# Optimization experiments

Hardware: AMD Instinct MI355X
Metric: run time of the kernel (lower is better)

## Reference

```python
import jax, jax.numpy as jnp
import numpy as np

B, N, CIN, COUT = 2, 4096, 128, 64

def setup_inputs() -> dict:
    key = jax.random.key(0)
    ks = jax.random.split(key, 9)
    s1 = 1.0 / np.sqrt(CIN)
    s2 = 1.0 / np.sqrt(COUT)
    sa = 1.0 / np.sqrt(2 * COUT)
    return {
        "x": jax.random.normal(ks[0], (B, N, CIN), dtype=jnp.float32),
        "adj_matrix": jax.random.uniform(ks[1], (B, N, N), dtype=jnp.float32),
        "W1": jax.random.uniform(ks[2], (CIN, COUT), jnp.float32, -s1, s1),
        "b1": jax.random.uniform(ks[3], (COUT,), jnp.float32, -s1, s1),
        "W2": jax.random.uniform(ks[4], (COUT, COUT), jnp.float32, -s2, s2),
        "b2": jax.random.uniform(ks[5], (COUT,), jnp.float32, -s2, s2),
        "Wa": jax.random.uniform(ks[6], (2 * COUT, 1), jnp.float32, -sa, sa),
        "ba": jax.random.uniform(ks[7], (1,), jnp.float32, -sa, sa),
    }

def reference(x, adj_matrix, W1, b1, W2, b2, Wa, ba):
    # conv: two Linear+ReLU layers -> h [B,N,C]
    h = jax.nn.relu(jnp.einsum('bni,io->bno', x, W1) + b1)
    h = jax.nn.relu(jnp.einsum('bni,io->bno', h, W2) + b2)
    # attention Linear(2C,1) on cat[h_i, h_j] factorizes: e_ij = sigmoid(u_i + v_j + b)
    C = h.shape[-1]
    u = jnp.einsum('bnc,c->bn', h, Wa[:C, 0])  # contribution of node i (row)
    v = jnp.einsum('bnc,c->bn', h, Wa[C:, 0])  # contribution of node j (col)
    e = jax.nn.sigmoid(u[:, :, None] + v[:, None, :] + ba[0])  # [B,N,N]
    a = e * adj_matrix
    a = a / (jnp.sum(a, axis=-1, keepdims=True) + 1e-10)
    h_out = jnp.einsum('bnm,bmc->bnc', a, h)
    return (h_out, a)
```

## Files before the change

### kernel.cpp

```cpp
#include <hip/hip_runtime.h>

#define BB 2
#define NN 4096
#define CIN 128
#define CC 64

typedef __attribute__((ext_vector_type(4))) float floatx4;
typedef __attribute__((ext_vector_type(8))) short short8;

__device__ __forceinline__ short f2bf(float f) {
    unsigned u = __float_as_uint(f);
    u += 0x7fffu + ((u >> 16) & 1u);
    return (short)(u >> 16);
}

__device__ __forceinline__ float sigf(float x) {
    return __builtin_amdgcn_rcpf(1.0f + __expf(-x));
}

__global__ __launch_bounds__(256) void feat_v3(
    const float* __restrict__ x, const float* __restrict__ W1,
    const float* __restrict__ b1, const float* __restrict__ W2,
    const float* __restrict__ b2, const float* __restrict__ Wa,
    const float* __restrict__ ba,
    short* __restrict__ hT, float* __restrict__ u, float* __restrict__ v)
{
    __shared__ float W1s[CIN * CC];
    __shared__ float W2s[CC * CC];
    __shared__ float xs[16 * 132];
    __shared__ float h1s[16 * 68];
    __shared__ __align__(16) short hs[CC][16];

    const int t = threadIdx.x;
    const int row0 = blockIdx.x * 16;

    {
        const floatx4* s1 = (const floatx4*)W1;
        floatx4* d1 = (floatx4*)W1s;
        for (int i = t; i < CIN * CC / 4; i += 256) d1[i] = s1[i];
        const floatx4* s2 = (const floatx4*)W2;
        floatx4* d2 = (floatx4*)W2s;
        for (int i = t; i < CC * CC / 4; i += 256) d2[i] = s2[i];
        const floatx4* sx = (const floatx4*)(x + (size_t)row0 * CIN);
        for (int i = t; i < 16 * CIN / 4; i += 256) {
            int rw = i >> 5, c4 = i & 31;
            *(floatx4*)(xs + rw * 132 + c4 * 4) = sx[i];
        }
    }
    __syncthreads();

    const int n  = t >> 4;
    const int cg = t & 15;
    const int c0 = cg * 4;

    float acc[4];
#pragma unroll
    for (int i = 0; i < 4; i++) acc[i] = b1[c0 + i];
    for (int k = 0; k < CIN; k++) {
        float a = xs[n * 132 + k];
        const floatx4 w = *(const floatx4*)&W1s[k * CC + c0];
#pragma unroll
        for (int i = 0; i < 4; i++) acc[i] = fmaf(a, w[i], acc[i]);
    }
#pragma unroll
    for (int i = 0; i < 4; i++) h1s[n * 68 + c0 + i] = fmaxf(acc[i], 0.0f);
    __syncthreads();

    float acc2[4];
#pragma unroll
    for (int i = 0; i < 4; i++) acc2[i] = b2[c0 + i];
    for (int k = 0; k < CC; k++) {
        float a = h1s[n * 68 + k];
        const floatx4 w = *(const floatx4*)&W2s[k * CC + c0];
#pragma unroll
        for (int i = 0; i < 4; i++) acc2[i] = fmaf(a, w[i], acc2[i]);
    }
#pragma unroll
    for (int i = 0; i < 4; i++) acc2[i] = fmaxf(acc2[i], 0.0f);

#pragma unroll
    for (int i = 0; i < 4; i++) hs[c0 + i][n] = f2bf(acc2[i]);

    float pu = 0.0f, pv = 0.0f;
#pragma unroll
    for (int i = 0; i < 4; i++) {
        pu = fmaf(acc2[i], Wa[c0 + i], pu);
        pv = fmaf(acc2[i], Wa[CC + c0 + i], pv);
    }
    pu += __shfl_down(pu, 8, 16); pv += __shfl_down(pv, 8, 16);
    pu += __shfl_down(pu, 4, 16); pv += __shfl_down(pv, 4, 16);
    pu += __shfl_down(pu, 2, 16); pv += __shfl_down(pv, 2, 16);
    pu += __shfl_down(pu, 1, 16); pv += __shfl_down(pv, 1, 16);

    const int grow = row0 + n;
    if (cg == 0) { u[grow] = pu + ba[0]; v[grow] = pv; }

    __syncthreads();
    if (t < 128) {
        const int c  = t >> 1;
        const int hf = t & 1;
        const int b   = row0 >> 12;
        const int nn0 = row0 & (NN - 1);
        *(short8*)(hT + ((size_t)(b * CC + c)) * NN + nn0 + hf * 8) =
            *(const short8*)&hs[c][hf * 8];
    }
}

__global__ __launch_bounds__(256, 2) void attn_v3(
    const float* __restrict__ adj, const float* __restrict__ u,
    const float* __restrict__ v, const short* __restrict__ hT,
    float* __restrict__ hout, float* __restrict__ aout)
{
    __shared__ float red[4][16][CC + 1];
    __shared__ float rsum[4][16];
    __shared__ float rinv[16];

    const int wave = threadIdx.x >> 6;
    const int lane = threadIdx.x & 63;
    const int row0 = blockIdx.x * 16;
    const int b  = row0 >> 12;
    const int n0 = row0 & (NN - 1);
    const float* vb = v + b * NN;
    const int jw = wave * 1024;

    float psum[16];
    {
        floatx4 vA = *(const floatx4*)(vb + jw +       lane * 4);
        floatx4 vB = *(const floatx4*)(vb + jw + 256 + lane * 4);
        floatx4 vC = *(const floatx4*)(vb + jw + 512 + lane * 4);
        floatx4 vD = *(const floatx4*)(vb + jw + 768 + lane * 4);
#pragma unroll 4
        for (int r = 0; r < 16; ++r) {
            const float* ar = adj + ((size_t)(b * NN + n0 + r)) * NN + jw;
            floatx4 aA = *(const floatx4*)(ar +       lane * 4);
            floatx4 aB = *(const floatx4*)(ar + 256 + lane * 4);
            floatx4 aC = *(const floatx4*)(ar + 512 + lane * 4);
            floatx4 aD = *(const floatx4*)(ar + 768 + lane * 4);
            const float ur = u[b * NN + n0 + r];
            float p = 0.f;
#pragma unroll
            for (int i = 0; i < 4; ++i) {
                p = fmaf(aA[i], sigf(ur + vA[i]), p);
                p = fmaf(aB[i], sigf(ur + vB[i]), p);
                p = fmaf(aC[i], sigf(ur + vC[i]), p);
                p = fmaf(aD[i], sigf(ur + vD[i]), p);
            }
            psum[r] = p;
        }
    }
#pragma unroll
    for (int off = 32; off; off >>= 1) {
#pragma unroll
        for (int r = 0; r < 16; ++r) psum[r] += __shfl_down(psum[r], off);
    }
    if (lane == 0) {
#pragma unroll
        for (int r = 0; r < 16; ++r) rsum[wave][r] = psum[r];
    }
    __syncthreads();
    if (threadIdx.x < 16) {
        const int r = threadIdx.x;
        float s = rsum[0][r] + rsum[1][r] + rsum[2][r] + rsum[3][r];
        rinv[r] = __builtin_amdgcn_rcpf(s + 1e-10f);
    }
    __syncthreads();

    const int quad = lane >> 4;
    const int m16  = lane & 15;
    const int n    = n0 + m16;
    const size_t rowbase = ((size_t)(b * NN + n)) * NN;
    const float un    = u[b * NN + n];
    const float inv_r = rinv[m16];

    const float* ap_base = adj + rowbase;
    float*       op_base = aout + rowbase;
    const short* hp0 = hT + ((size_t)(b * CC +  0 + m16)) * NN;
    const short* hp1 = hT + ((size_t)(b * CC + 16 + m16)) * NN;
    const short* hp2 = hT + ((size_t)(b * CC + 32 + m16)) * NN;
    const short* hp3 = hT + ((size_t)(b * CC + 48 + m16)) * NN;

    floatx4 acc[4];
#pragma unroll
    for (int g = 0; g < 4; g++) acc[g] = (floatx4){0.f, 0.f, 0.f, 0.f};

    const int jb0 = jw + quad * 8;

    floatx4 a0A, a1A, v0A, v1A; short8 h0A, h1A, h2A, h3A;
    floatx4 a0B, a1B, v0B, v1B; short8 h0B, h1B, h2B, h3B;

#define LOADST(S, jb) { \
    a0##S = *(const floatx4*)(ap_base + (jb));      \
    a1##S = *(const floatx4*)(ap_base + (jb) + 4);  \
    v0##S = *(const floatx4*)(vb + (jb));           \
    v1##S = *(const floatx4*)(vb + (jb) + 4);       \
    h0##S = *(const short8*)(hp0 + (jb));           \
    h1##S = *(const short8*)(hp1 + (jb));           \
    h2##S = *(const short8*)(hp2 + (jb));           \
    h3##S = *(const short8*)(hp3 + (jb)); }

#define COMPST(S, jb) { \
    float av[8] = {a0##S.x, a0##S.y, a0##S.z, a0##S.w, a1##S.x, a1##S.y, a1##S.z, a1##S.w}; \
    float vv[8] = {v0##S.x, v0##S.y, v0##S.z, v0##S.w, v1##S.x, v1##S.y, v1##S.z, v1##S.w}; \
    floatx4 o0, o1; short8 af; \
    _Pragma("unroll") \
    for (int i = 0; i < 8; ++i) { \
        float s_ = av[i] * sigf(un + vv[i]) * inv_r; \
        if (i < 4) o0[i] = s_; else o1[i - 4] = s_; \
        af[i] = f2bf(s_); } \
    __builtin_nontemporal_store(o0, (floatx4*)(op_base + (jb)));     \
    __builtin_nontemporal_store(o1, (floatx4*)(op_base + (jb) + 4)); \
    acc[0] = __builtin_amdgcn_mfma_f32_16x16x32_bf16(af, h0##S, acc[0], 0, 0, 0); \
    acc[1] = __builtin_amdgcn_mfma_f32_16x16x32_bf16(af, h1##S, acc[1], 0, 0, 0); \
    acc[2] = __builtin_amdgcn_mfma_f32_16x16x32_bf16(af, h2##S, acc[2], 0, 0, 0); \
    acc[3] = __builtin_amdgcn_mfma_f32_16x16x32_bf16(af, h3##S, acc[3], 0, 0, 0); }

    LOADST(A, jb0)
    LOADST(B, jb0 + 32)
#pragma unroll
    for (int s = 0; s < 32; s += 2) {
        COMPST(A, jb0 + s * 32)
        if (s + 2 < 32) LOADST(A, jb0 + (s + 2) * 32)
        COMPST(B, jb0 + (s + 1) * 32)
        if (s + 3 < 32) LOADST(B, jb0 + (s + 3) * 32)
    }
#undef LOADST
#undef COMPST

#pragma unroll
    for (int g = 0; g < 4; g++) {
        const int c = g * 16 + m16;
#pragma unroll
        for (int i = 0; i < 4; i++)
            red[wave][quad * 4 + i][c] = acc[g][i];
    }
    __syncthreads();

#pragma unroll
    for (int e = 0; e < 4; e++) {
        const int idx = threadIdx.x * 4 + e;
        const int rr = idx >> 6;
        const int c  = idx & 63;
        float s = red[0][rr][c] + red[1][rr][c] + red[2][rr][c] + red[3][rr][c];
        hout[((size_t)(b * NN + n0 + rr)) * CC + c] = s;
    }
}

extern "C" void kernel_launch(void* const* d_in, const int* in_sizes, int n_in,
                              void* d_out, int out_size, void* d_ws, size_t ws_size,
                              hipStream_t stream) {
    (void)in_sizes; (void)n_in; (void)out_size; (void)ws_size;
    const float* x   = (const float*)d_in[0];
    const float* adj = (const float*)d_in[1];
    const float* W1  = (const float*)d_in[2];
    const float* b1  = (const float*)d_in[3];
    const float* W2  = (const float*)d_in[4];
    const float* b2  = (const float*)d_in[5];
    const float* Wa  = (const float*)d_in[6];
    const float* ba  = (const float*)d_in[7];

    float* hout = (float*)d_out;
    float* aout = hout + (size_t)BB * NN * CC;

    char* ws = (char*)d_ws;
    short* hT = (short*)ws;
    float* u  = (float*)(ws + (size_t)BB * CC * NN * sizeof(short));
    float* vv = u + BB * NN;

    feat_v3<<<BB * NN / 16, 256, 0, stream>>>(x, W1, b1, W2, b2, Wa, ba, hT, u, vv);
    attn_v3<<<BB * NN / 16, 256, 0, stream>>>(adj, u, vv, hT, hout, aout);
}
```

Measured before the change: 300.0 us.

## Restructure attention kernel: per-wave row pairs, LDS-staged bf16 tiles, split-K MFMA

```diff
diff --git a/kernel.cpp b/kernel.cpp
--- a/kernel.cpp
+++ b/kernel.cpp
@@ -4,9 +4,12 @@
 #define NN 4096
 #define CIN 128
 #define CC 64
+#define JT 256
+#define NTILES (NN / JT)
 
 typedef __attribute__((ext_vector_type(4))) float floatx4;
 typedef __attribute__((ext_vector_type(8))) short short8;
+typedef __attribute__((ext_vector_type(4))) short short4v;
 
 __device__ __forceinline__ short f2bf(float f) {
     unsigned u = __float_as_uint(f);
@@ -16,6 +19,11 @@
 
 __device__ __forceinline__ float sigf(float x) {
     return __builtin_amdgcn_rcpf(1.0f + __expf(-x));
+}
+
+__device__ __forceinline__ void lbar() {
+    asm volatile("s_waitcnt lgkmcnt(0)" ::: "memory");
+    __builtin_amdgcn_s_barrier();
 }
 
 __global__ __launch_bounds__(256) void feat_v3(
@@ -106,142 +114,110 @@
     }
 }
 
-__global__ __launch_bounds__(256, 2) void attn_v3(
+__global__ __launch_bounds__(512, 4) void attn_v4(
     const float* __restrict__ adj, const float* __restrict__ u,
     const float* __restrict__ v, const short* __restrict__ hT,
     float* __restrict__ hout, float* __restrict__ aout)
 {
-    __shared__ float red[4][16][CC + 1];
-    __shared__ float rsum[4][16];
-    __shared__ float rinv[16];
+    __shared__ __align__(16) short P[2][16][264];
+    __shared__ float red[4][16][17];
 
     const int wave = threadIdx.x >> 6;
     const int lane = threadIdx.x & 63;
+    const int quad = lane >> 4;
+    const int m16  = lane & 15;
+
     const int row0 = blockIdx.x * 16;
     const int b  = row0 >> 12;
     const int n0 = row0 & (NN - 1);
     const float* vb = v + b * NN;
-    const int jw = wave * 1024;
-
-    float psum[16];
-    {
-        floatx4 vA = *(const floatx4*)(vb + jw +       lane * 4);
-        floatx4 vB = *(const floatx4*)(vb + jw + 256 + lane * 4);
-        floatx4 vC = *(const floatx4*)(vb + jw + 512 + lane * 4);
-        floatx4 vD = *(const floatx4*)(vb + jw + 768 + lane * 4);
+
+    const int r0 = 2 * wave;
+    const float u0 = u[b * NN + n0 + r0];
+    const float u1 = u[b * NN + n0 + r0 + 1];
+    const float* a0p = adj + ((size_t)(b * NN + n0 + r0)) * NN;
+    const float* a1p = a0p + NN;
+    float* o0p = aout + ((size_t)(b * NN + n0 + r0)) * NN;
+    float* o1p = o0p + NN;
+
+    float s0 = 0.f, s1 = 0.f;
 #pragma unroll 4
-        for (int r = 0; r < 16; ++r) {
-            const float* ar = adj + ((size_t)(b * NN + n0 + r)) * NN + jw;
-            floatx4 aA = *(const floatx4*)(ar +       lane * 4);
-            floatx4 aB = *(const floatx4*)(ar + 256 + lane * 4);
-            floatx4 aC = *(const floatx4*)(ar + 512 + lane * 4);
-            floatx4 aD = *(const floatx4*)(ar + 768 + lane * 4);
-            const float ur = u[b * NN + n0 + r];
-            float p = 0.f;
-#pragma unroll
-            for (int i = 0; i < 4; ++i) {
-                p = fmaf(aA[i], sigf(ur + vA[i]), p);
-                p = fmaf(aB[i], sigf(ur + vB[i]), p);
-                p = fmaf(aC[i], sigf(ur + vC[i]), p);
-                p = fmaf(aD[i], sigf(ur + vD[i]), p);
-            }
-            psum[r] = p;
+    for (int c = 0; c < 16; ++c) {
+        const int j = c * 256 + lane * 4;
+        const floatx4 va = *(const floatx4*)(vb + j);
+        const floatx4 aa = *(const floatx4*)(a0p + j);
+        const floatx4 ab = *(const floatx4*)(a1p + j);
+#pragma unroll
+        for (int i = 0; i < 4; ++i) {
+            s0 = fmaf(aa[i], sigf(u0 + va[i]), s0);
+            s1 = fmaf(ab[i], sigf(u1 + va[i]), s1);
         }
     }
 #pragma unroll
     for (int off = 32; off; off >>= 1) {
-#pragma unroll
-        for (int r = 0; r < 16; ++r) psum[r] += __shfl_down(psum[r], off);
-    }
-    if (lane == 0) {
-#pragma unroll
-        for (int r = 0; r < 16; ++r) rsum[wave][r] = psum[r];
-    }
-    __syncthreads();
-    if (threadIdx.x < 16) {
-        const int r = threadIdx.x;
-        float s = rsum[0][r] + rsum[1][r] + rsum[2][r] + rsum[3][r];
-        rinv[r] = __builtin_amdgcn_rcpf(s + 1e-10f);
-    }
-    __syncthreads();
-
-    const int quad = lane >> 4;
-    const int m16  = lane & 15;
-    const int n    = n0 + m16;
-    const size_t rowbase = ((size_t)(b * NN + n)) * NN;
-    const float un    = u[b * NN + n];
-    const float inv_r = rinv[m16];
-
-    const float* ap_base = adj + rowbase;
-    float*       op_base = aout + rowbase;
-    const short* hp0 = hT + ((size_t)(b * CC +  0 + m16)) * NN;
-    const short* hp1 = hT + ((size_t)(b * CC + 16 + m16)) * NN;
-    const short* hp2 = hT + ((size_t)(b * CC + 32 + m16)) * NN;
-    const short* hp3 = hT + ((size_t)(b * CC + 48 + m16)) * NN;
-
-    floatx4 acc[4];
-#pragma unroll
-    for (int g = 0; g < 4; g++) acc[g] = (floatx4){0.f, 0.f, 0.f, 0.f};
-
-    const int jb0 = jw + quad * 8;
-
-    floatx4 a0A, a1A, v0A, v1A; short8 h0A, h1A, h2A, h3A;
-    floatx4 a0B, a1B, v0B, v1B; short8 h0B, h1B, h2B, h3B;
-
-#define LOADST(S, jb) { \
-    a0##S = *(const floatx4*)(ap_base + (jb));      \
-    a1##S = *(const floatx4*)(ap_base + (jb) + 4);  \
-    v0##S = *(const floatx4*)(vb + (jb));           \
-    v1##S = *(const floatx4*)(vb + (jb) + 4);       \
-    h0##S = *(const short8*)(hp0 + (jb));           \
-    h1##S = *(const short8*)(hp1 + (jb));           \
-    h2##S = *(const short8*)(hp2 + (jb));           \
-    h3##S = *(const short8*)(hp3 + (jb)); }
-
-#define COMPST(S, jb) { \
-    float av[8] = {a0##S.x, a0##S.y, a0##S.z, a0##S.w, a1##S.x, a1##S.y, a1##S.z, a1##S.w}; \
-    float vv[8] = {v0##S.x, v0##S.y, v0##S.z, v0##S.w, v1##S.x, v1##S.y, v1##S.z, v1##S.w}; \
-    floatx4 o0, o1; short8 af; \
+        s0 += __shfl_down(s0, off);
+        s1 += __shfl_down(s1, off);
+    }
+    s0 = __shfl(s0, 0);
+    s1 = __shfl(s1, 0);
+    const float ir0 = __builtin_amdgcn_rcpf(s0 + 1e-10f);
+    const float ir1 = __builtin_amdgcn_rcpf(s1 + 1e-10f);
+
+    const int c0 = (wave & 3) * 16;
+    const int kh = wave >> 2;
+    const short* hp = hT + ((size_t)(b * CC + c0 + m16)) * NN;
+
+    floatx4 acc = (floatx4){0.f, 0.f, 0.f, 0.f};
+
+#define FILL(T, BUF) { \
+    const int j = (T) * JT + lane * 4; \
+    const floatx4 va = *(const floatx4*)(vb + j); \
+    const floatx4 aa = *(const floatx4*)(a0p + j); \
+    const floatx4 ab = *(const floatx4*)(a1p + j); \
+    floatx4 o0, o1; short4v pk0, pk1; \
     _Pragma("unroll") \
-    for (int i = 0; i < 8; ++i) { \
-        float s_ = av[i] * sigf(un + vv[i]) * inv_r; \
-        if (i < 4) o0[i] = s_; else o1[i - 4] = s_; \
-        af[i] = f2bf(s_); } \
-    __builtin_nontemporal_store(o0, (floatx4*)(op_base + (jb)));     \
-    __builtin_nontemporal_store(o1, (floatx4*)(op_base + (jb) + 4)); \
-    acc[0] = __builtin_amdgcn_mfma_f32_16x16x32_bf16(af, h0##S, acc[0], 0, 0, 0); \
-    acc[1] = __builtin_amdgcn_mfma_f32_16x16x32_bf16(af, h1##S, acc[1], 0, 0, 0); \
-    acc[2] = __builtin_amdgcn_mfma_f32_16x16x32_bf16(af, h2##S, acc[2], 0, 0, 0); \
-    acc[3] = __builtin_amdgcn_mfma_f32_16x16x32_bf16(af, h3##S, acc[3], 0, 0, 0); }
-
-    LOADST(A, jb0)
-    LOADST(B, jb0 + 32)
-#pragma unroll
-    for (int s = 0; s < 32; s += 2) {
-        COMPST(A, jb0 + s * 32)
-        if (s + 2 < 32) LOADST(A, jb0 + (s + 2) * 32)
-        COMPST(B, jb0 + (s + 1) * 32)
-        if (s + 3 < 32) LOADST(B, jb0 + (s + 3) * 32)
-    }
-#undef LOADST
-#undef COMPST
-
-#pragma unroll
-    for (int g = 0; g < 4; g++) {
-        const int c = g * 16 + m16;
-#pragma unroll
-        for (int i = 0; i < 4; i++)
-            red[wave][quad * 4 + i][c] = acc[g][i];
-    }
-    __syncthreads();
-
-#pragma unroll
-    for (int e = 0; e < 4; e++) {
-        const int idx = threadIdx.x * 4 + e;
-        const int rr = idx >> 6;
-        const int c  = idx & 63;
-        float s = red[0][rr][c] + red[1][rr][c] + red[2][rr][c] + red[3][rr][c];
-        hout[((size_t)(b * NN + n0 + rr)) * CC + c] = s;
+    for (int i = 0; i < 4; ++i) { \
+        float sA = aa[i] * sigf(u0 + va[i]) * ir0; \
+        float sB = ab[i] * sigf(u1 + va[i]) * ir1; \
+        o0[i] = sA; o1[i] = sB; \
+        pk0[i] = f2bf(sA); pk1[i] = f2bf(sB); } \
+    __builtin_nontemporal_store(o0, (floatx4*)(o0p + j)); \
+    __builtin_nontemporal_store(o1, (floatx4*)(o1p + j)); \
+    *(short4v*)&P[BUF][r0][lane * 4]     = pk0; \
+    *(short4v*)&P[BUF][r0 + 1][lane * 4] = pk1; }
+
+#define MM(T, BUF) { \
+    const short* hpt = hp + (size_t)(T) * JT; \
+    _Pragma("unroll") \
+    for (int ks = 0; ks < 4; ++ks) { \
+        const int kk = kh * 4 + ks; \
+        const short8 Af = *(const short8*)&P[BUF][m16][kk * 32 + quad * 8]; \
+        const short8 Bf = *(const short8*)(hpt + kk * 32 + quad * 8); \
+        acc = __builtin_amdgcn_mfma_f32_16x16x32_bf16(Af, Bf, acc, 0, 0, 0); \
+    } }
+
+    FILL(0, 0)
+    lbar();
+#pragma unroll 2
+    for (int t = 0; t < NTILES; ++t) {
+        if (t + 1 < NTILES) { FILL(t + 1, (t + 1) & 1) }
+        MM(t, t & 1)
+        lbar();
+    }
+#undef FILL
+#undef MM
+
+    if (kh == 1) {
+#pragma unroll
+        for (int i = 0; i < 4; ++i) red[wave - 4][quad * 4 + i][m16] = acc[i];
+    }
+    __syncthreads();
+    if (kh == 0) {
+#pragma unroll
+        for (int i = 0; i < 4; ++i) {
+            const float sfin = acc[i] + red[wave][quad * 4 + i][m16];
+            hout[((size_t)(b * NN + n0 + quad * 4 + i)) * CC + c0 + m16] = sfin;
+        }
     }
 }
 
@@ -267,5 +243,5 @@
     float* vv = u + BB * NN;
 
     feat_v3<<<BB * NN / 16, 256, 0, stream>>>(x, W1, b1, W2, b2, Wa, ba, hT, u, vv);
-    attn_v3<<<BB * NN / 16, 256, 0, stream>>>(adj, u, vv, hT, hout, aout);
-}
+    attn_v4<<<BB * NN / 16, 512, 0, stream>>>(adj, u, vv, hT, hout, aout);
+}
```

Result: faster. 289.7 us (-3.4%).

## Split row-sum into separate kernel and split attention columns across blocks with atomics

Applied to the files above, without the earlier changes.

```diff
diff --git a/kernel.cpp b/kernel.cpp
--- a/kernel.cpp
+++ b/kernel.cpp
@@ -106,72 +106,59 @@
     }
 }
 
-__global__ __launch_bounds__(256, 2) void attn_v3(
+__global__ __launch_bounds__(256) void rowsum_v2(
     const float* __restrict__ adj, const float* __restrict__ u,
-    const float* __restrict__ v, const short* __restrict__ hT,
+    const float* __restrict__ v, float* __restrict__ r)
+{
+    const int wave = threadIdx.x >> 6;
+    const int lane = threadIdx.x & 63;
+    const int row  = blockIdx.x * 4 + wave;
+    const int b = row >> 12;
+    const float un = u[row];
+    const floatx4* arow = (const floatx4*)(adj + (size_t)row * NN);
+    const floatx4* vb = (const floatx4*)(v + b * NN);
+
+    float p0 = 0.f, p1 = 0.f, p2 = 0.f, p3 = 0.f;
+#pragma unroll 4
+    for (int i = 0; i < 16; i++) {
+        int idx = lane + i * 64;
+        floatx4 a4 = arow[idx];
+        floatx4 v4 = vb[idx];
+        p0 = fmaf(a4.x, sigf(un + v4.x), p0);
+        p1 = fmaf(a4.y, sigf(un + v4.y), p1);
+        p2 = fmaf(a4.z, sigf(un + v4.z), p2);
+        p3 = fmaf(a4.w, sigf(un + v4.w), p3);
+    }
+    float p = (p0 + p1) + (p2 + p3);
+#pragma unroll
+    for (int off = 32; off > 0; off >>= 1) p += __shfl_down(p, off);
+    if (lane == 0) r[row] = p;
+}
+
+__global__ __launch_bounds__(256, 4) void attn_v6(
+    const float* __restrict__ adj, const float* __restrict__ u,
+    const float* __restrict__ v, const float* __restrict__ r,
+    const short* __restrict__ hT,
     float* __restrict__ hout, float* __restrict__ aout)
 {
     __shared__ float red[4][16][CC + 1];
-    __shared__ float rsum[4][16];
-    __shared__ float rinv[16];
 
     const int wave = threadIdx.x >> 6;
     const int lane = threadIdx.x & 63;
-    const int row0 = blockIdx.x * 16;
+    const int quad = lane >> 4;
+    const int m16  = lane & 15;
+
+    const int tile = blockIdx.x >> 2;
+    const int jq   = blockIdx.x & 3;
+    const int row0 = tile * 16;
     const int b  = row0 >> 12;
     const int n0 = row0 & (NN - 1);
-    const float* vb = v + b * NN;
-    const int jw = wave * 1024;
-
-    float psum[16];
-    {
-        floatx4 vA = *(const floatx4*)(vb + jw +       lane * 4);
-        floatx4 vB = *(const floatx4*)(vb + jw + 256 + lane * 4);
-        floatx4 vC = *(const floatx4*)(vb + jw + 512 + lane * 4);
-        floatx4 vD = *(const floatx4*)(vb + jw + 768 + lane * 4);
-#pragma unroll 4
-        for (int r = 0; r < 16; ++r) {
-            const float* ar = adj + ((size_t)(b * NN + n0 + r)) * NN + jw;
-            floatx4 aA = *(const floatx4*)(ar +       lane * 4);
-            floatx4 aB = *(const floatx4*)(ar + 256 + lane * 4);
-            floatx4 aC = *(const floatx4*)(ar + 512 + lane * 4);
-            floatx4 aD = *(const floatx4*)(ar + 768 + lane * 4);
-            const float ur = u[b * NN + n0 + r];
-            float p = 0.f;
-#pragma unroll
-            for (int i = 0; i < 4; ++i) {
-                p = fmaf(aA[i], sigf(ur + vA[i]), p);
-                p = fmaf(aB[i], sigf(ur + vB[i]), p);
-                p = fmaf(aC[i], sigf(ur + vC[i]), p);
-                p = fmaf(aD[i], sigf(ur + vD[i]), p);
-            }
-            psum[r] = p;
-        }
-    }
-#pragma unroll
-    for (int off = 32; off; off >>= 1) {
-#pragma unroll
-        for (int r = 0; r < 16; ++r) psum[r] += __shfl_down(psum[r], off);
-    }
-    if (lane == 0) {
-#pragma unroll
-        for (int r = 0; r < 16; ++r) rsum[wave][r] = psum[r];
-    }
-    __syncthreads();
-    if (threadIdx.x < 16) {
-        const int r = threadIdx.x;
-        float s = rsum[0][r] + rsum[1][r] + rsum[2][r] + rsum[3][r];
-        rinv[r] = __builtin_amdgcn_rcpf(s + 1e-10f);
-    }
-    __syncthreads();
-
-    const int quad = lane >> 4;
-    const int m16  = lane & 15;
-    const int n    = n0 + m16;
+    const int n  = n0 + m16;
+
     const size_t rowbase = ((size_t)(b * NN + n)) * NN;
     const float un    = u[b * NN + n];
-    const float inv_r = rinv[m16];
-
+    const float inv_r = __builtin_amdgcn_rcpf(r[b * NN + n] + 1e-10f);
+    const float* vb = v + b * NN;
     const float* ap_base = adj + rowbase;
     float*       op_base = aout + rowbase;
     const short* hp0 = hT + ((size_t)(b * CC +  0 + m16)) * NN;
@@ -183,7 +170,7 @@
 #pragma unroll
     for (int g = 0; g < 4; g++) acc[g] = (floatx4){0.f, 0.f, 0.f, 0.f};
 
-    const int jb0 = jw + quad * 8;
+    const int jb0 = jq * 1024 + wave * 256 + quad * 8;
 
     floatx4 a0A, a1A, v0A, v1A; short8 h0A, h1A, h2A, h3A;
     floatx4 a0B, a1B, v0B, v1B; short8 h0B, h1B, h2B, h3B;
@@ -217,11 +204,11 @@
     LOADST(A, jb0)
     LOADST(B, jb0 + 32)
 #pragma unroll
-    for (int s = 0; s < 32; s += 2) {
+    for (int s = 0; s < 8; s += 2) {
         COMPST(A, jb0 + s * 32)
-        if (s + 2 < 32) LOADST(A, jb0 + (s + 2) * 32)
+        if (s + 2 < 8) LOADST(A, jb0 + (s + 2) * 32)
         COMPST(B, jb0 + (s + 1) * 32)
-        if (s + 3 < 32) LOADST(B, jb0 + (s + 3) * 32)
+        if (s + 3 < 8) LOADST(B, jb0 + (s + 3) * 32)
     }
 #undef LOADST
 #undef COMPST
@@ -241,7 +228,7 @@
         const int rr = idx >> 6;
         const int c  = idx & 63;
         float s = red[0][rr][c] + red[1][rr][c] + red[2][rr][c] + red[3][rr][c];
-        hout[((size_t)(b * NN + n0 + rr)) * CC + c] = s;
+        atomicAdd(&hout[((size_t)(b * NN + n0 + rr)) * CC + c], s);
     }
 }
 
@@ -265,7 +252,10 @@
     short* hT = (short*)ws;
     float* u  = (float*)(ws + (size_t)BB * CC * NN * sizeof(short));
     float* vv = u + BB * NN;
-
+    float* r  = vv + BB * NN;
+
+    hipMemsetAsync(hout, 0, (size_t)BB * NN * CC * sizeof(float), stream);
     feat_v3<<<BB * NN / 16, 256, 0, stream>>>(x, W1, b1, W2, b2, Wa, ba, hT, u, vv);
-    attn_v3<<<BB * NN / 16, 256, 0, stream>>>(adj, u, vv, hT, hout, aout);
-}
+    rowsum_v2<<<BB * NN / 4, 256, 0, stream>>>(adj, u, vv, r);
+    attn_v6<<<(BB * NN / 16) * 4, 256, 0, stream>>>(adj, u, vv, r, hT, hout, aout);
+}
```

Measured after the change: 310.8 us. 1.04x slower.
